# Optimization experiments

Hardware: AMD Instinct MI355X
Metric: run time of the kernel (lower is better)

Reference implementation:

```python
import jax, jax.numpy as jnp
import numpy as np
from jax import lax

S = 224          # raster_settings.image_size
K = 10           # raster_settings.faces_per_pixel
BLUR = 1e-4      # raster_settings.blur_radius (signed squared-dist threshold)
SIGMA = 1e-4     # BlendParams().sigma used by sigmoid_alpha_blend
BIG = 1e10
AREA_EPS = 1e-10


def setup_inputs():
    key = jax.random.key(0)
    k1, k2, k3 = jax.random.split(key, 3)
    B, V, F = 2, 5023, 5000
    xy = jax.random.uniform(k1, (B, V, 2), minval=-1.0, maxval=1.0)
    z = jax.random.uniform(k2, (B, V, 1), minval=0.5, maxval=1.5)
    vertices = jnp.concatenate([xy, z], -1).astype(jnp.float32)
    faces = jax.random.randint(k3, (B, F, 3), 0, V, dtype=jnp.int32)
    return {"vertices": vertices, "faces": faces}


def _cross2(a, b):
    return a[..., 0] * b[..., 1] - a[..., 1] * b[..., 0]


def _edge_d2(a, b, p):
    # squared distance from points p [W,1,2] to segment (a,b) [F,2] -> [W,F]
    ab = b - a
    ap = p - a
    t = jnp.clip((ap * ab).sum(-1) / jnp.maximum((ab * ab).sum(-1), 1e-12), 0.0, 1.0)
    proj = a + t[..., None] * ab
    return ((p - proj) ** 2).sum(-1)


def _rasterize_one(verts, faces):
    # naive PyTorch3D-style rasterizer for one mesh: per pixel, keep K nearest
    # faces (by interpolated z) whose signed squared dist to the triangle < BLUR.
    tri = verts[faces]                                  # [F,3,3]
    v0, v1, v2 = tri[:, 0, :2], tri[:, 1, :2], tri[:, 2, :2]
    z0, z1, z2 = tri[:, 0, 2], tri[:, 1, 2], tri[:, 2, 2]
    area = _cross2(v1 - v0, v2 - v0)
    good_face = jnp.abs(area) > AREA_EPS                # cull degenerate faces
    area_safe = jnp.where(good_face, area, 1.0)
    # NDC pixel centers (pytorch3d convention: +x left, +y up; verts pre-negated)
    coords = 1.0 - (2.0 * jnp.arange(S, dtype=verts.dtype) + 1.0) / S

    def row(yf):
        p = jnp.stack([coords, jnp.full((S,), yf, verts.dtype)], -1)[:, None, :]  # [W,1,2]
        w0 = _cross2(v2 - v1, p - v1) / area_safe       # [W,F] barycentric
        w1 = _cross2(v0 - v2, p - v2) / area_safe
        w2 = _cross2(v1 - v0, p - v0) / area_safe
        z = w0 * z0 + w1 * z1 + w2 * z2                  # no perspective correction (default)
        inside = (w0 > 0) & (w1 > 0) & (w2 > 0)
        d2 = jnp.minimum(jnp.minimum(_edge_d2(v0, v1, p), _edge_d2(v1, v2, p)),
                         _edge_d2(v2, v0, p))
        sd = jnp.where(inside, -d2, d2)                  # signed squared dist
        valid = good_face & (z > 0) & (sd <= BLUR)
        negz = jnp.where(valid, -z, -BIG)
        vals, idx = lax.top_k(negz, K)                   # K nearest by z
        vk = vals > -0.5 * BIG
        zk = jnp.take_along_axis(z, idx, -1)
        dk = jnp.take_along_axis(sd, idx, -1)
        return (jnp.where(vk, idx, -1), jnp.where(vk, zk, -1.0), jnp.where(vk, dk, -1.0))

    return lax.map(row, coords)                          # each [S,S,K]


def reference(vertices, faces):
    B, V, _ = vertices.shape
    F = faces.shape[1]
    fixed = vertices * jnp.array([-1.0, -1.0, 1.0], vertices.dtype)  # flip x,y (DECA)
    p2f_l, zbuf, dists = jax.vmap(_rasterize_one)(fixed, faces)      # [B,S,S,K]
    mask = p2f_l >= 0
    # packed (global) pix_to_face like pytorch3d
    p2f = jnp.where(mask, p2f_l + (jnp.arange(B) * F)[:, None, None, None], -1)
    # sigmoid_alpha_blend: alpha = 1 - prod(1 - sigmoid(-dist/sigma))
    prob = jax.nn.sigmoid(-dists / SIGMA) * mask
    alpha = 1.0 - jnp.prod(1.0 - prob, -1)               # [B,S,S]
    images = alpha[:, None, :, :]                        # images[...,3:].permute(0,3,1,2)
    # vertex visibility from nearest face per pixel (scatter)
    faces_packed = (faces + V * jnp.arange(B, dtype=faces.dtype)[:, None, None]).reshape(-1, 3)
    faces_all = jnp.concatenate([faces_packed, -jnp.ones((1, 3), faces.dtype)], 0)
    vis_verts = faces_all[p2f[..., 0].reshape(-1)].reshape(-1)  # -1 wraps to sentinel row
    vv = jnp.zeros(B * V + 1, vertices.dtype).at[vis_verts].set(1.0)
    visibility = vv[:-1].reshape(B, V)                   # extra slot absorbs -1 indices
    return images, visibility
```

## Files before the change

### kernel.cpp

```cpp
#include <hip/hip_runtime.h>
#include <math.h>

#define SDIM 224
#define KTOP 10
#define NB 2
#define NV 5023
#define NF 5000
#define FSTB 24
#define BLUR 1e-4f
#define IMG_SZ (NB * SDIM * SDIM)
#define NW 8
#define SEG (NF / NW)
#define CAP 1024
#define HT 0.031251f
#define COV_THR 0.04422f
#define REL_THR (-0.0543f)

__device__ __forceinline__ float seg_d2_exact(float ax, float ay, float abx, float aby,
                                              float L, float px, float py) {
    float apx = __fsub_rn(px, ax), apy = __fsub_rn(py, ay);
    float dot = __fadd_rn(__fmul_rn(apx, abx), __fmul_rn(apy, aby));
    float t = __fdiv_rn(dot, L);
    t = fminf(fmaxf(t, 0.0f), 1.0f);
    float prx = __fadd_rn(ax, __fmul_rn(t, abx));
    float pry = __fadd_rn(ay, __fmul_rn(t, aby));
    float dx = __fsub_rn(px, prx), dy = __fsub_rn(py, pry);
    return __fadd_rn(__fmul_rn(dx, dx), __fmul_rn(dy, dy));
}

__global__ void preprocess_kernel(const float* __restrict__ verts,
                                  const int* __restrict__ faces,
                                  float4* __restrict__ fdA,
                                  float* __restrict__ fdB,
                                  float4* __restrict__ fdC,
                                  float* __restrict__ out)
{
    const int idx = blockIdx.x * blockDim.x + threadIdx.x;
    if (idx < NB * NV) out[IMG_SZ + idx] = 0.0f;
    if (idx >= NB * NF) return;
    const int b = idx / NF;
    const int* fp = faces + (size_t)idx * 3;
    const int i0 = fp[0], i1 = fp[1], i2 = fp[2];
    const float* vb = verts + (size_t)b * NV * 3;
    const float v0x = -vb[i0*3+0], v0y = -vb[i0*3+1], z0 = vb[i0*3+2];
    const float v1x = -vb[i1*3+0], v1y = -vb[i1*3+1], z1 = vb[i1*3+2];
    const float v2x = -vb[i2*3+0], v2y = -vb[i2*3+1], z2 = vb[i2*3+2];
    const float e01x = __fsub_rn(v1x, v0x), e01y = __fsub_rn(v1y, v0y);
    const float e12x = __fsub_rn(v2x, v1x), e12y = __fsub_rn(v2y, v1y);
    const float e20x = __fsub_rn(v0x, v2x), e20y = __fsub_rn(v0y, v2y);
    const float area = __fsub_rn(__fmul_rn(e01x, __fsub_rn(v2y, v0y)),
                                 __fmul_rn(e01y, __fsub_rn(v2x, v0x)));
    const bool good = fabsf(area) > 1e-10f;
    const float area_safe = good ? area : 1.0f;
    const float L01 = fmaxf(__fadd_rn(__fmul_rn(e01x,e01x), __fmul_rn(e01y,e01y)), 1e-12f);
    const float L12 = fmaxf(__fadd_rn(__fmul_rn(e12x,e12x), __fmul_rn(e12y,e12y)), 1e-12f);
    const float L20 = fmaxf(__fadd_rn(__fmul_rn(e20x,e20x), __fmul_rn(e20y,e20y)), 1e-12f);

    double Zx = 0.0, Zy = 0.0, Zc = 0.0;
    float mgc = 0.0f, ccx = 0.0f, ccy = 0.0f, RR = -1.0f;
    float n0x=0,n0y=0,n0c=-3e38f, n1x=0,n1y=0,n1c=-3e38f, n2x=0,n2y=0,n2c=-3e38f;
    if (good) {
        const double invA = 1.0 / (double)area;
        const double c0c = (double)e12y*v1x - (double)e12x*v1y;
        const double c1c = (double)e20y*v2x - (double)e20x*v2y;
        const double c2c = (double)e01y*v0x - (double)e01x*v0y;
        Zx = (-(double)e12y*z0 - (double)e20y*z1 - (double)e01y*z2) * invA;
        Zy = ( (double)e12x*z0 + (double)e20x*z1 + (double)e01x*z2) * invA;
        Zc = (c0c*z0 + c1c*z1 + c2c*z2) * invA;
        const double B0 = fabs((double)e12x)*(1.0+fabs((double)v1y)) + fabs((double)e12y)*(1.0+fabs((double)v1x));
        const double B1 = fabs((double)e20x)*(1.0+fabs((double)v2y)) + fabs((double)e20y)*(1.0+fabs((double)v2x));
        const double B2 = fabs((double)e01x)*(1.0+fabs((double)v0y)) + fabs((double)e01y)*(1.0+fabs((double)v0x));
        const double B = (B0*(double)z0 + B1*(double)z1 + B2*(double)z2) * fabs(invA);
        mgc = (float)(2.5e-6 * B) + 1e-20f;
        const double cx = ((double)v0x + (double)v1x + (double)v2x) / 3.0;
        const double cy = ((double)v0y + (double)v1y + (double)v2y) / 3.0;
        const double d0 = (v0x-cx)*(v0x-cx) + (v0y-cy)*(v0y-cy);
        const double d1 = (v1x-cx)*(v1x-cx) + (v1y-cy)*(v1y-cy);
        const double d2 = (v2x-cx)*(v2x-cx) + (v2y-cy)*(v2y-cy);
        const double R = sqrt(fmax(d0, fmax(d1, d2))) + 0.0111;
        ccx = (float)cx; ccy = (float)cy;
        RR = (float)(R * R) * 1.0001f;
        const double s = (area > 0.0f) ? 1.0 : -1.0;
        const double l12 = sqrt((double)e12x*e12x + (double)e12y*e12y);
        const double l20 = sqrt((double)e20x*e20x + (double)e20y*e20y);
        const double l01 = sqrt((double)e01x*e01x + (double)e01y*e01y);
        const double i12 = s / fmax(l12, 1e-300);
        const double i20 = s / fmax(l20, 1e-300);
        const double i01 = s / fmax(l01, 1e-300);
        n0x = (float)(-(double)e12y * i12);
        n0y = (float)( (double)e12x * i12);
        n0c = (float)(((double)e12y*v1x - (double)e12x*v1y) * i12);
        n1x = (float)(-(double)e20y * i20);
        n1y = (float)( (double)e20x * i20);
        n1c = (float)(((double)e20y*v2x - (double)e20x*v2y) * i20);
        n2x = (float)(-(double)e01y * i01);
        n2y = (float)( (double)e01x * i01);
        n2c = (float)(((double)e01y*v0x - (double)e01x*v0y) * i01);
    }
    fdA[2*idx]   = make_float4((float)Zx, (float)Zy, (float)Zc, mgc);
    fdA[2*idx+1] = make_float4(ccx, ccy, RR, 0.0f);
    fdC[3*idx+0] = make_float4(n0x, n0y, n0c, n1x);
    fdC[3*idx+1] = make_float4(n1y, n1c, n2x, n2y);
    fdC[3*idx+2] = make_float4(n2c, 0.0f, 0.0f, 0.0f);
    float* q = fdB + (size_t)idx * FSTB;
    q[0]=v0x;  q[1]=v0y;  q[2]=v1x;  q[3]=v1y;  q[4]=v2x;  q[5]=v2y;
    q[6]=e01x; q[7]=e01y; q[8]=e12x; q[9]=e12y; q[10]=e20x; q[11]=e20y;
    q[12]=z0;  q[13]=z1;  q[14]=z2;  q[15]=area_safe;
    q[16]=L01; q[17]=L12; q[18]=L20;
    q[19]=__fdiv_rn(1.0f, L01); q[20]=__fdiv_rn(1.0f, L12); q[21]=__fdiv_rn(1.0f, L20);
    q[22]=0.0f; q[23]=0.0f;
}

__global__ __launch_bounds__(64 * NW) void raster_kernel(const float4* __restrict__ fdA,
                                                         const float* __restrict__ fdB,
                                                         const float4* __restrict__ fdC,
                                                         const int* __restrict__ faces,
                                                         float* __restrict__ out)
{
    const int b = blockIdx.z;
    const int lane = threadIdx.x & 63;
    const int w = __builtin_amdgcn_readfirstlane((int)(threadIdx.x >> 6));
    const int x = (blockIdx.x << 3) + (lane & 7);
    const int y = (blockIdx.y << 3) + (lane >> 3);
    const float px = __fsub_rn(1.0f, __fdiv_rn(__fadd_rn(__fmul_rn(2.0f, (float)x), 1.0f), (float)SDIM));
    const float py = __fsub_rn(1.0f, __fdiv_rn(__fadd_rn(__fmul_rn(2.0f, (float)y), 1.0f), (float)SDIM));
    const float pcx = __fsub_rn(1.0f, __fdiv_rn((float)(16 * blockIdx.x + 8), 224.0f));
    const float pcy = __fsub_rn(1.0f, __fdiv_rn((float)(16 * blockIdx.y + 8), 224.0f));

    __shared__ int   sList[CAP];
    __shared__ int   sHist[64];
    __shared__ int   sCnt[NW];
    __shared__ int   sOff[NW];
    __shared__ int   sLen;
    __shared__ float sT;
    __shared__ float sZ[NW][64][11];
    __shared__ float sS[NW][64][11];
    __shared__ float sBZ[NW][64];
    __shared__ int   sBI[NW][64];

    if (threadIdx.x < 64) sHist[threadIdx.x] = 0;
    __syncthreads();

    const float4* __restrict__ fa = fdA + (size_t)b * NF * 2;
    const float*  __restrict__ fb = fdB + (size_t)b * NF * FSTB;
    const float4* __restrict__ fc = fdC + (size_t)b * NF * 3;

    const int f0 = w * SEG, f1 = f0 + SEG;
    float dm[10], zl[10], zh[10];
#pragma unroll
    for (int it = 0; it < 10; ++it) {
        const int f = f0 + it * 64 + lane;
        dm[it] = -3e38f; zl[it] = 3e38f; zh[it] = -3e38f;
        if (f < f1) {
            const float4 a0 = fa[2*f];
            const float4 cA = fc[3*f+0];
            const float4 cB = fc[3*f+1];
            const float4 cC = fc[3*f+2];
            const float d0 = fmaf(cA.x, pcx, fmaf(cA.y, pcy, cA.z));
            const float d1 = fmaf(cA.w, pcx, fmaf(cB.x, pcy, cB.y));
            const float d2 = fmaf(cB.z, pcx, fmaf(cB.w, pcy, cC.x));
            const float dmin = fminf(d0, fminf(d1, d2));
            const float ztc = fmaf(a0.x, pcx, fmaf(a0.y, pcy, a0.z));
            const float spread = fmaf(fabsf(a0.x), HT, fmaf(fabsf(a0.y), HT, 2.0f * a0.w)) + 1e-6f;
            dm[it] = dmin; zl[it] = ztc - spread; zh[it] = ztc + spread;
            if ((dmin >= COV_THR) && (zl[it] > 0.0f)) {
                int bk = (int)floorf((zh[it] - 0.4f) * 53.333332f);
                bk = max(0, min(63, bk));
                atomicAdd(&sHist[bk], 1);
            }
        }
    }
    __syncthreads();

    if (threadIdx.x == 0) {
        int cum = 0; float T = 3e38f;
        for (int k2 = 0; k2 < 64; ++k2) {
            cum += sHist[k2];
            if (cum >= KTOP) { T = (k2 >= 63) ? 3e38f : (0.4f + (float)(k2+1) * 0.01875f + 1e-4f); break; }
        }
        sT = T;
    }
    __syncthreads();
    const float Tt = sT;

    int svMask = 0, cnt = 0;
#pragma unroll
    for (int it = 0; it < 10; ++it) {
        const bool sv = (dm[it] >= REL_THR) && (zl[it] <= Tt) && (zh[it] > 0.0f);
        if (sv) svMask |= (1 << it);
        cnt += (int)__popcll(__ballot(sv));
    }
    if (lane == 0) sCnt[w] = cnt;
    __syncthreads();
    if (threadIdx.x == 0) {
        int acc = 0;
        for (int w2 = 0; w2 < NW; ++w2) { sOff[w2] = acc; acc += sCnt[w2]; }
        sLen = (acc <= CAP) ? acc : -1;
    }
    __syncthreads();
    const int Ltot = sLen;

    if (Ltot >= 0) {
        const unsigned long long below = ((lane == 63) ? ~0ull : ((1ull << (lane + 1)) - 1ull)) >> 1;
        int woff = sOff[w];
#pragma unroll
        for (int it = 0; it < 10; ++it) {
            const bool sv = (svMask >> it) & 1;
            const unsigned long long m = __ballot(sv);
            if (sv) sList[woff + (int)__popcll(m & below)] = f0 + it * 64 + lane;
            woff += (int)__popcll(m);
        }
    }
    __syncthreads();

    float tz[KTOP], ts[KTOP];
#pragma unroll
    for (int j = 0; j < KTOP; ++j) { tz[j] = 3e38f; ts[j] = 3e38f; }
    float bestZ = 3e38f;
    int bestIdx = -1;

    int jbeg, jend;
    if (Ltot >= 0) {
        const int chunk = (Ltot + NW - 1) / NW;
        jbeg = w * chunk; jend = min(Ltot, jbeg + chunk);
    } else {
        jbeg = f0; jend = f1;
    }
    for (int j = jbeg; j < jend; ++j) {
        const int f = (Ltot >= 0) ? __builtin_amdgcn_readfirstlane(sList[j]) : j;
        const float4 aA = fa[2*f];
        const float4 aB = fa[2*f+1];
        const float zt  = fmaf(aA.x, px, fmaf(aA.y, py, aA.z));
        const float dcx = px - aB.x, dcy = py - aB.y;
        const float d2c = fmaf(dcx, dcx, dcy*dcy);
        const float thr = tz[KTOP-1];
        const bool pass = (d2c <= aB.z) & (zt > -aA.w) & (zt < thr + aA.w);
        if (!__any(pass)) continue;

        const float* q = fb + (size_t)f * FSTB;
        const float v0x=q[0], v0y=q[1], v1x=q[2], v1y=q[3], v2x=q[4], v2y=q[5];
        const float e01x=q[6], e01y=q[7], e12x=q[8], e12y=q[9], e20x=q[10], e20y=q[11];
        const float z0=q[12], z1=q[13], z2=q[14], area=q[15];
        const float L01=q[16], L12=q[17], L20=q[18];
        const float il01=q[19], il12=q[20], il20=q[21];
        if (!pass) continue;

        const float c0 = __fsub_rn(__fmul_rn(e12x, __fsub_rn(py, v1y)),
                                   __fmul_rn(e12y, __fsub_rn(px, v1x)));
        const float c1 = __fsub_rn(__fmul_rn(e20x, __fsub_rn(py, v2y)),
                                   __fmul_rn(e20y, __fsub_rn(px, v2x)));
        const float c2 = __fsub_rn(__fmul_rn(e01x, __fsub_rn(py, v0y)),
                                   __fmul_rn(e01y, __fsub_rn(px, v0x)));

        const bool ap = area > 0.0f;
        const bool s0 = ap ? (c0 > 0.0f) : (c0 < 0.0f);
        const bool s1 = ap ? (c1 > 0.0f) : (c1 < 0.0f);
        const bool s2 = ap ? (c2 > 0.0f) : (c2 < 0.0f);
        if (!(s0 & s1 & s2)) {
            float r = 0.0f;
            if (!s0) r = fmaxf(r, c0 * c0 * il12);
            if (!s1) r = fmaxf(r, c1 * c1 * il20);
            if (!s2) r = fmaxf(r, c2 * c2 * il01);
            if (r > BLUR * 1.0001f) continue;
        }

        const float w0 = __fdiv_rn(c0, area);
        const float w1 = __fdiv_rn(c1, area);
        const float w2 = __fdiv_rn(c2, area);
        const float z = __fadd_rn(__fadd_rn(__fmul_rn(w0, z0), __fmul_rn(w1, z1)),
                                  __fmul_rn(w2, z2));
        if (!(z > 0.0f)) continue;
        if (!(z < tz[KTOP-1])) continue;

        const bool inside = (w0 > 0.0f) & (w1 > 0.0f) & (w2 > 0.0f);
        float sd;
        if (inside) {
            const float mld = fminf(fminf(c0*c0*il12, c1*c1*il20), c2*c2*il01);
            if (mld >= 1e-3f) {
                sd = -1.0f;
            } else {
                const float d2 = fminf(fminf(
                    seg_d2_exact(v0x, v0y, e01x, e01y, L01, px, py),
                    seg_d2_exact(v1x, v1y, e12x, e12y, L12, px, py)),
                    seg_d2_exact(v2x, v2y, e20x, e20y, L20, px, py));
                sd = -d2;
            }
        } else {
            const float d2 = fminf(fminf(
                seg_d2_exact(v0x, v0y, e01x, e01y, L01, px, py),
                seg_d2_exact(v1x, v1y, e12x, e12y, L12, px, py)),
                seg_d2_exact(v2x, v2y, e20x, e20y, L20, px, py));
            if (!(d2 <= BLUR)) continue;
            sd = d2;
        }

        if (z < bestZ) { bestZ = z; bestIdx = f; }

        float cz = z, cs = sd;
#pragma unroll
        for (int j2 = 0; j2 < KTOP; ++j2) {
            if (cz < tz[j2]) {
                const float oz = tz[j2], os = ts[j2];
                tz[j2] = cz; ts[j2] = cs; cz = oz; cs = os;
            }
        }
    }

#pragma unroll
    for (int j = 0; j < KTOP; ++j) { sZ[w][lane][j] = tz[j]; sS[w][lane][j] = ts[j]; }
    sZ[w][lane][KTOP] = 3e38f;
    sBZ[w][lane] = bestZ;
    sBI[w][lane] = bestIdx;
    __syncthreads();

    if (threadIdx.x < 64) {
        const int p = threadIdx.x;
        float bz = sBZ[0][p]; int bi = sBI[0][p];
#pragma unroll
        for (int w2 = 1; w2 < NW; ++w2) {
            if (sBZ[w2][p] < bz) { bz = sBZ[w2][p]; bi = sBI[w2][p]; }
        }
        int ptr[NW];
#pragma unroll
        for (int w2 = 0; w2 < NW; ++w2) ptr[w2] = 0;
        float prod = 1.0f;
#pragma unroll
        for (int k = 0; k < KTOP; ++k) {
            float mz = 3e38f; int mw = -1;
#pragma unroll
            for (int w2 = 0; w2 < NW; ++w2) {
                const float zc = sZ[w2][p][ptr[w2]];
                if (zc < mz) { mz = zc; mw = w2; }
            }
            float sd = 3e38f;
#pragma unroll
            for (int w2 = 0; w2 < NW; ++w2) {
                if (w2 == mw) { sd = sS[w2][p][ptr[w2]]; ptr[w2]++; }
            }
            prod *= 1.0f / (1.0f + __expf(-sd * 1e4f));
        }
        const float alpha = 1.0f - prod;
        const int gx = (blockIdx.x << 3) + (p & 7);
        const int gy = (blockIdx.y << 3) + (p >> 3);
        out[(size_t)b * (SDIM * SDIM) + gy * SDIM + gx] = alpha;

        if (bi >= 0) {
            const int* fp = faces + ((size_t)b * NF + bi) * 3;
            float* vis = out + IMG_SZ;
            vis[b * NV + fp[0]] = 1.0f;
            vis[b * NV + fp[1]] = 1.0f;
            vis[b * NV + fp[2]] = 1.0f;
        }
    }
}

extern "C" void kernel_launch(void* const* d_in, const int* in_sizes, int n_in,
                              void* d_out, int out_size, void* d_ws, size_t ws_size,
                              hipStream_t stream)
{
    const float* verts = (const float*)d_in[0];
    const int*   faces = (const int*)d_in[1];
    float* out = (float*)d_out;
    float4* fdA = (float4*)d_ws;
    float*  fdB = (float*)((char*)d_ws + NB * NF * 32);
    float4* fdC = (float4*)((char*)d_ws + NB * NF * (32 + 96));

    const int total = NB * NV;
    preprocess_kernel<<<dim3((total + 255) / 256), dim3(256), 0, stream>>>(verts, faces, fdA, fdB, fdC, out);
    raster_kernel<<<dim3(SDIM / 8, SDIM / 8, NB), dim3(64 * NW), 0, stream>>>(fdA, fdB, fdC, faces, out);
}
```

Baseline: 189.5 us.

## Compact per-face data, prefetch next face, recompute edges in heavy path

Per-face records shrink from 24 floats plus a centroid record to three float4 vertex/z records and one float4 depth-plane record. Edge vectors and lengths are now recomputed in a separate heavy_face helper, and the bounding-circle test is dropped. The compact loop software-prefetches the next face's data one iteration ahead, and launch bounds now request 6 blocks per SM. The goal is less memory traffic and load latency per face, paid for with extra ALU work per candidate and a weaker early cull.

```diff
diff --git a/kernel.cpp b/kernel.cpp
--- a/kernel.cpp
+++ b/kernel.cpp
@@ -6,7 +6,6 @@
 #define NB 2
 #define NV 5023
 #define NF 5000
-#define FSTB 24
 #define BLUR 1e-4f
 #define IMG_SZ (NB * SDIM * SDIM)
 #define NW 8
@@ -30,9 +29,9 @@
 
 __global__ void preprocess_kernel(const float* __restrict__ verts,
                                   const int* __restrict__ faces,
-                                  float4* __restrict__ fdA,
-                                  float* __restrict__ fdB,
-                                  float4* __restrict__ fdC,
+                                  float4* __restrict__ ga,
+                                  float4* __restrict__ hh,
+                                  float4* __restrict__ cc,
                                   float* __restrict__ out)
 {
     const int idx = blockIdx.x * blockDim.x + threadIdx.x;
@@ -52,12 +51,9 @@
                                  __fmul_rn(e01y, __fsub_rn(v2x, v0x)));
     const bool good = fabsf(area) > 1e-10f;
     const float area_safe = good ? area : 1.0f;
-    const float L01 = fmaxf(__fadd_rn(__fmul_rn(e01x,e01x), __fmul_rn(e01y,e01y)), 1e-12f);
-    const float L12 = fmaxf(__fadd_rn(__fmul_rn(e12x,e12x), __fmul_rn(e12y,e12y)), 1e-12f);
-    const float L20 = fmaxf(__fadd_rn(__fmul_rn(e20x,e20x), __fmul_rn(e20y,e20y)), 1e-12f);
 
     double Zx = 0.0, Zy = 0.0, Zc = 0.0;
-    float mgc = 0.0f, ccx = 0.0f, ccy = 0.0f, RR = -1.0f;
+    float mgc = -1.0f;
     float n0x=0,n0y=0,n0c=-3e38f, n1x=0,n1y=0,n1c=-3e38f, n2x=0,n2y=0,n2c=-3e38f;
     if (good) {
         const double invA = 1.0 / (double)area;
@@ -72,14 +68,6 @@
         const double B2 = fabs((double)e01x)*(1.0+fabs((double)v0y)) + fabs((double)e01y)*(1.0+fabs((double)v0x));
         const double B = (B0*(double)z0 + B1*(double)z1 + B2*(double)z2) * fabs(invA);
         mgc = (float)(2.5e-6 * B) + 1e-20f;
-        const double cx = ((double)v0x + (double)v1x + (double)v2x) / 3.0;
-        const double cy = ((double)v0y + (double)v1y + (double)v2y) / 3.0;
-        const double d0 = (v0x-cx)*(v0x-cx) + (v0y-cy)*(v0y-cy);
-        const double d1 = (v1x-cx)*(v1x-cx) + (v1y-cy)*(v1y-cy);
-        const double d2 = (v2x-cx)*(v2x-cx) + (v2y-cy)*(v2y-cy);
-        const double R = sqrt(fmax(d0, fmax(d1, d2))) + 0.0111;
-        ccx = (float)cx; ccy = (float)cy;
-        RR = (float)(R * R) * 1.0001f;
         const double s = (area > 0.0f) ? 1.0 : -1.0;
         const double l12 = sqrt((double)e12x*e12x + (double)e12y*e12y);
         const double l20 = sqrt((double)e20x*e20x + (double)e20y*e20y);
@@ -97,25 +85,100 @@
         n2y = (float)( (double)e01x * i01);
         n2c = (float)(((double)e01y*v0x - (double)e01x*v0y) * i01);
     }
-    fdA[2*idx]   = make_float4((float)Zx, (float)Zy, (float)Zc, mgc);
-    fdA[2*idx+1] = make_float4(ccx, ccy, RR, 0.0f);
-    fdC[3*idx+0] = make_float4(n0x, n0y, n0c, n1x);
-    fdC[3*idx+1] = make_float4(n1y, n1c, n2x, n2y);
-    fdC[3*idx+2] = make_float4(n2c, 0.0f, 0.0f, 0.0f);
-    float* q = fdB + (size_t)idx * FSTB;
-    q[0]=v0x;  q[1]=v0y;  q[2]=v1x;  q[3]=v1y;  q[4]=v2x;  q[5]=v2y;
-    q[6]=e01x; q[7]=e01y; q[8]=e12x; q[9]=e12y; q[10]=e20x; q[11]=e20y;
-    q[12]=z0;  q[13]=z1;  q[14]=z2;  q[15]=area_safe;
-    q[16]=L01; q[17]=L12; q[18]=L20;
-    q[19]=__fdiv_rn(1.0f, L01); q[20]=__fdiv_rn(1.0f, L12); q[21]=__fdiv_rn(1.0f, L20);
-    q[22]=0.0f; q[23]=0.0f;
-}
-
-__global__ __launch_bounds__(64 * NW) void raster_kernel(const float4* __restrict__ fdA,
-                                                         const float* __restrict__ fdB,
-                                                         const float4* __restrict__ fdC,
-                                                         const int* __restrict__ faces,
-                                                         float* __restrict__ out)
+    ga[idx]     = make_float4((float)Zx, (float)Zy, (float)Zc, mgc);
+    cc[3*idx+0] = make_float4(n0x, n0y, n0c, n1x);
+    cc[3*idx+1] = make_float4(n1y, n1c, n2x, n2y);
+    cc[3*idx+2] = make_float4(n2c, 0.0f, 0.0f, 0.0f);
+    hh[3*idx+0] = make_float4(v0x, v0y, v1x, v1y);
+    hh[3*idx+1] = make_float4(v2x, v2y, z0, z1);
+    hh[3*idx+2] = make_float4(z2, area_safe, 0.0f, 0.0f);
+}
+
+__device__ __forceinline__ void heavy_face(float4 h0, float4 h1, float4 h2,
+                                           int fidx, bool pass, float px, float py,
+                                           float tz[KTOP], float ts[KTOP],
+                                           float& bestZ, int& bestIdx)
+{
+    if (!pass) return;
+    const float v0x=h0.x, v0y=h0.y, v1x=h0.z, v1y=h0.w;
+    const float v2x=h1.x, v2y=h1.y, z0=h1.z, z1=h1.w;
+    const float z2=h2.x, area=h2.y;
+    const float e01x = __fsub_rn(v1x, v0x), e01y = __fsub_rn(v1y, v0y);
+    const float e12x = __fsub_rn(v2x, v1x), e12y = __fsub_rn(v2y, v1y);
+    const float e20x = __fsub_rn(v0x, v2x), e20y = __fsub_rn(v0y, v2y);
+
+    const float c0 = __fsub_rn(__fmul_rn(e12x, __fsub_rn(py, v1y)),
+                               __fmul_rn(e12y, __fsub_rn(px, v1x)));
+    const float c1 = __fsub_rn(__fmul_rn(e20x, __fsub_rn(py, v2y)),
+                               __fmul_rn(e20y, __fsub_rn(px, v2x)));
+    const float c2 = __fsub_rn(__fmul_rn(e01x, __fsub_rn(py, v0y)),
+                               __fmul_rn(e01y, __fsub_rn(px, v0x)));
+
+    const float L01 = fmaxf(__fadd_rn(__fmul_rn(e01x,e01x), __fmul_rn(e01y,e01y)), 1e-12f);
+    const float L12 = fmaxf(__fadd_rn(__fmul_rn(e12x,e12x), __fmul_rn(e12y,e12y)), 1e-12f);
+    const float L20 = fmaxf(__fadd_rn(__fmul_rn(e20x,e20x), __fmul_rn(e20y,e20y)), 1e-12f);
+
+    const bool ap = area > 0.0f;
+    const bool s0 = ap ? (c0 > 0.0f) : (c0 < 0.0f);
+    const bool s1 = ap ? (c1 > 0.0f) : (c1 < 0.0f);
+    const bool s2 = ap ? (c2 > 0.0f) : (c2 < 0.0f);
+    if (!(s0 & s1 & s2)) {
+        bool cull = false;
+        if (!s0) cull |= (c0 * c0 > BLUR * 1.0002f * L12);
+        if (!s1) cull |= (c1 * c1 > BLUR * 1.0002f * L20);
+        if (!s2) cull |= (c2 * c2 > BLUR * 1.0002f * L01);
+        if (cull) return;
+    }
+
+    const float w0 = __fdiv_rn(c0, area);
+    const float w1 = __fdiv_rn(c1, area);
+    const float w2 = __fdiv_rn(c2, area);
+    const float z = __fadd_rn(__fadd_rn(__fmul_rn(w0, z0), __fmul_rn(w1, z1)),
+                              __fmul_rn(w2, z2));
+    if (!(z > 0.0f)) return;
+    if (!(z < tz[KTOP-1])) return;
+
+    const bool inside = (w0 > 0.0f) & (w1 > 0.0f) & (w2 > 0.0f);
+    float sd;
+    if (inside) {
+        const bool sat = (c0*c0 >= 1.0002e-3f * L12) &
+                         (c1*c1 >= 1.0002e-3f * L20) &
+                         (c2*c2 >= 1.0002e-3f * L01);
+        if (sat) {
+            sd = -1.0f;
+        } else {
+            const float d2 = fminf(fminf(
+                seg_d2_exact(v0x, v0y, e01x, e01y, L01, px, py),
+                seg_d2_exact(v1x, v1y, e12x, e12y, L12, px, py)),
+                seg_d2_exact(v2x, v2y, e20x, e20y, L20, px, py));
+            sd = -d2;
+        }
+    } else {
+        const float d2 = fminf(fminf(
+            seg_d2_exact(v0x, v0y, e01x, e01y, L01, px, py),
+            seg_d2_exact(v1x, v1y, e12x, e12y, L12, px, py)),
+            seg_d2_exact(v2x, v2y, e20x, e20y, L20, px, py));
+        if (!(d2 <= BLUR)) return;
+        sd = d2;
+    }
+
+    if (z < bestZ) { bestZ = z; bestIdx = fidx; }
+
+    float cz = z, cs = sd;
+#pragma unroll
+    for (int j = 0; j < KTOP; ++j) {
+        if (cz < tz[j]) {
+            const float oz = tz[j], os = ts[j];
+            tz[j] = cz; ts[j] = cs; cz = oz; cs = os;
+        }
+    }
+}
+
+__global__ __launch_bounds__(64 * NW, 6) void raster_kernel(const float4* __restrict__ gaG,
+                                                            const float4* __restrict__ hhG,
+                                                            const float4* __restrict__ ccG,
+                                                            const int* __restrict__ faces,
+                                                            float* __restrict__ out)
 {
     const int b = blockIdx.z;
     const int lane = threadIdx.x & 63;
@@ -141,9 +204,9 @@
     if (threadIdx.x < 64) sHist[threadIdx.x] = 0;
     __syncthreads();
 
-    const float4* __restrict__ fa = fdA + (size_t)b * NF * 2;
-    const float*  __restrict__ fb = fdB + (size_t)b * NF * FSTB;
-    const float4* __restrict__ fc = fdC + (size_t)b * NF * 3;
+    const float4* __restrict__ ga = gaG + (size_t)b * NF;
+    const float4* __restrict__ hh = hhG + (size_t)b * NF * 3;
+    const float4* __restrict__ cc = ccG + (size_t)b * NF * 3;
 
     const int f0 = w * SEG, f1 = f0 + SEG;
     float dm[10], zl[10], zh[10];
@@ -152,18 +215,18 @@
         const int f = f0 + it * 64 + lane;
         dm[it] = -3e38f; zl[it] = 3e38f; zh[it] = -3e38f;
         if (f < f1) {
-            const float4 a0 = fa[2*f];
-            const float4 cA = fc[3*f+0];
-            const float4 cB = fc[3*f+1];
-            const float4 cC = fc[3*f+2];
+            const float4 a0 = ga[f];
+            const float4 cA = cc[3*f+0];
+            const float4 cB = cc[3*f+1];
+            const float4 cC = cc[3*f+2];
             const float d0 = fmaf(cA.x, pcx, fmaf(cA.y, pcy, cA.z));
             const float d1 = fmaf(cA.w, pcx, fmaf(cB.x, pcy, cB.y));
             const float d2 = fmaf(cB.z, pcx, fmaf(cB.w, pcy, cC.x));
             const float dmin = fminf(d0, fminf(d1, d2));
             const float ztc = fmaf(a0.x, pcx, fmaf(a0.y, pcy, a0.z));
-            const float spread = fmaf(fabsf(a0.x), HT, fmaf(fabsf(a0.y), HT, 2.0f * a0.w)) + 1e-6f;
+            const float spread = fmaf(fabsf(a0.x), HT, fmaf(fabsf(a0.y), HT, 2.0f * fabsf(a0.w))) + 1e-6f;
             dm[it] = dmin; zl[it] = ztc - spread; zh[it] = ztc + spread;
-            if ((dmin >= COV_THR) && (zl[it] > 0.0f)) {
+            if ((a0.w > 0.0f) && (dmin >= COV_THR) && (zl[it] > 0.0f)) {
                 int bk = (int)floorf((zh[it] - 0.4f) * 53.333332f);
                 bk = max(0, min(63, bk));
                 atomicAdd(&sHist[bk], 1);
@@ -219,89 +282,37 @@
     float bestZ = 3e38f;
     int bestIdx = -1;
 
-    int jbeg, jend;
     if (Ltot >= 0) {
         const int chunk = (Ltot + NW - 1) / NW;
-        jbeg = w * chunk; jend = min(Ltot, jbeg + chunk);
+        const int jb = w * chunk, je = min(Ltot, jb + chunk);
+        if (jb < je) {
+            int fA = __builtin_amdgcn_readfirstlane(sList[jb]);
+            int fB = __builtin_amdgcn_readfirstlane(sList[min(jb + 1, je - 1)]);
+            float4 gC  = ga[fA];
+            float4 hC0 = hh[3*fA+0], hC1 = hh[3*fA+1], hC2 = hh[3*fA+2];
+            for (int j = jb; j < je; ++j) {
+                const int fN = __builtin_amdgcn_readfirstlane(sList[min(j + 2, je - 1)]);
+                const float4 gN  = ga[fB];
+                const float4 hN0 = hh[3*fB+0], hN1 = hh[3*fB+1], hN2 = hh[3*fB+2];
+                const float zt  = fmaf(gC.x, px, fmaf(gC.y, py, gC.z));
+                const float thr = tz[KTOP-1];
+                const bool pass = (zt > -gC.w) & (zt < thr + gC.w);
+                if (__any(pass)) {
+                    heavy_face(hC0, hC1, hC2, fA, pass, px, py, tz, ts, bestZ, bestIdx);
+                }
+                fA = fB; fB = fN;
+                gC = gN; hC0 = hN0; hC1 = hN1; hC2 = hN2;
+            }
+        }
     } else {
-        jbeg = f0; jend = f1;
-    }
-    for (int j = jbeg; j < jend; ++j) {
-        const int f = (Ltot >= 0) ? __builtin_amdgcn_readfirstlane(sList[j]) : j;
-        const float4 aA = fa[2*f];
-        const float4 aB = fa[2*f+1];
-        const float zt  = fmaf(aA.x, px, fmaf(aA.y, py, aA.z));
-        const float dcx = px - aB.x, dcy = py - aB.y;
-        const float d2c = fmaf(dcx, dcx, dcy*dcy);
-        const float thr = tz[KTOP-1];
-        const bool pass = (d2c <= aB.z) & (zt > -aA.w) & (zt < thr + aA.w);
-        if (!__any(pass)) continue;
-
-        const float* q = fb + (size_t)f * FSTB;
-        const float v0x=q[0], v0y=q[1], v1x=q[2], v1y=q[3], v2x=q[4], v2y=q[5];
-        const float e01x=q[6], e01y=q[7], e12x=q[8], e12y=q[9], e20x=q[10], e20y=q[11];
-        const float z0=q[12], z1=q[13], z2=q[14], area=q[15];
-        const float L01=q[16], L12=q[17], L20=q[18];
-        const float il01=q[19], il12=q[20], il20=q[21];
-        if (!pass) continue;
-
-        const float c0 = __fsub_rn(__fmul_rn(e12x, __fsub_rn(py, v1y)),
-                                   __fmul_rn(e12y, __fsub_rn(px, v1x)));
-        const float c1 = __fsub_rn(__fmul_rn(e20x, __fsub_rn(py, v2y)),
-                                   __fmul_rn(e20y, __fsub_rn(px, v2x)));
-        const float c2 = __fsub_rn(__fmul_rn(e01x, __fsub_rn(py, v0y)),
-                                   __fmul_rn(e01y, __fsub_rn(px, v0x)));
-
-        const bool ap = area > 0.0f;
-        const bool s0 = ap ? (c0 > 0.0f) : (c0 < 0.0f);
-        const bool s1 = ap ? (c1 > 0.0f) : (c1 < 0.0f);
-        const bool s2 = ap ? (c2 > 0.0f) : (c2 < 0.0f);
-        if (!(s0 & s1 & s2)) {
-            float r = 0.0f;
-            if (!s0) r = fmaxf(r, c0 * c0 * il12);
-            if (!s1) r = fmaxf(r, c1 * c1 * il20);
-            if (!s2) r = fmaxf(r, c2 * c2 * il01);
-            if (r > BLUR * 1.0001f) continue;
-        }
-
-        const float w0 = __fdiv_rn(c0, area);
-        const float w1 = __fdiv_rn(c1, area);
-        const float w2 = __fdiv_rn(c2, area);
-        const float z = __fadd_rn(__fadd_rn(__fmul_rn(w0, z0), __fmul_rn(w1, z1)),
-                                  __fmul_rn(w2, z2));
-        if (!(z > 0.0f)) continue;
-        if (!(z < tz[KTOP-1])) continue;
-
-        const bool inside = (w0 > 0.0f) & (w1 > 0.0f) & (w2 > 0.0f);
-        float sd;
-        if (inside) {
-            const float mld = fminf(fminf(c0*c0*il12, c1*c1*il20), c2*c2*il01);
-            if (mld >= 1e-3f) {
-                sd = -1.0f;
-            } else {
-                const float d2 = fminf(fminf(
-                    seg_d2_exact(v0x, v0y, e01x, e01y, L01, px, py),
-                    seg_d2_exact(v1x, v1y, e12x, e12y, L12, px, py)),
-                    seg_d2_exact(v2x, v2y, e20x, e20y, L20, px, py));
-                sd = -d2;
-            }
-        } else {
-            const float d2 = fminf(fminf(
-                seg_d2_exact(v0x, v0y, e01x, e01y, L01, px, py),
-                seg_d2_exact(v1x, v1y, e12x, e12y, L12, px, py)),
-                seg_d2_exact(v2x, v2y, e20x, e20y, L20, px, py));
-            if (!(d2 <= BLUR)) continue;
-            sd = d2;
-        }
-
-        if (z < bestZ) { bestZ = z; bestIdx = f; }
-
-        float cz = z, cs = sd;
-#pragma unroll
-        for (int j2 = 0; j2 < KTOP; ++j2) {
-            if (cz < tz[j2]) {
-                const float oz = tz[j2], os = ts[j2];
-                tz[j2] = cz; ts[j2] = cs; cz = oz; cs = os;
+        for (int f = f0; f < f1; ++f) {
+            const float4 g = ga[f];
+            const float zt  = fmaf(g.x, px, fmaf(g.y, py, g.z));
+            const float thr = tz[KTOP-1];
+            const bool pass = (zt > -g.w) & (zt < thr + g.w);
+            if (__any(pass)) {
+                heavy_face(hh[3*f+0], hh[3*f+1], hh[3*f+2], f, pass, px, py,
+                           tz, ts, bestZ, bestIdx);
             }
         }
     }
@@ -361,11 +372,11 @@
     const float* verts = (const float*)d_in[0];
     const int*   faces = (const int*)d_in[1];
     float* out = (float*)d_out;
-    float4* fdA = (float4*)d_ws;
-    float*  fdB = (float*)((char*)d_ws + NB * NF * 32);
-    float4* fdC = (float4*)((char*)d_ws + NB * NF * (32 + 96));
+    float4* ga = (float4*)d_ws;
+    float4* hh = (float4*)((char*)d_ws + NB * NF * 16);
+    float4* cc = (float4*)((char*)d_ws + NB * NF * (16 + 48));
 
     const int total = NB * NV;
-    preprocess_kernel<<<dim3((total + 255) / 256), dim3(256), 0, stream>>>(verts, faces, fdA, fdB, fdC, out);
-    raster_kernel<<<dim3(SDIM / 8, SDIM / 8, NB), dim3(64 * NW), 0, stream>>>(fdA, fdB, fdC, faces, out);
-}
+    preprocess_kernel<<<dim3((total + 255) / 256), dim3(256), 0, stream>>>(verts, faces, ga, hh, cc, out);
+    raster_kernel<<<dim3(SDIM / 8, SDIM / 8, NB), dim3(64 * NW), 0, stream>>>(ga, hh, cc, faces, out);
+}
```

New measurement: 191.7 us. Within noise of the previous version (+1.1%).
